# Kernel tuning notes

Hardware: AMD Instinct MI355X
Metric: run time of the kernel (lower is better)

The kernel has to match this reference:

```python
import jax, jax.numpy as jnp
import numpy as np

B, N, D = 256, 133, 1024
H, C = 8, 128  # per-head channels; H*C == out_channels
NEG_SLOPE = 0.2


def setup_inputs() -> dict:
    key = jax.random.key(0)
    kx, kw, ka, kadj = jax.random.split(key, 4)
    x = jax.random.normal(kx, (B, N, D), dtype=jnp.float32)
    W = jax.random.normal(kw, (H * C, D), dtype=jnp.float32) * 0.02  # nn.Linear weight (out,in)
    attn_w = jax.random.normal(ka, (2 * C,), dtype=jnp.float32) * 0.02  # attn Linear(2C,1) weight
    # binary adjacency with self-loops so every softmax column has a valid entry
    bern = (jax.random.uniform(kadj, (N, N)) < 0.15).astype(jnp.float32)
    adj = jnp.maximum(bern, jnp.eye(N, dtype=jnp.float32))[:, :, None]  # (N,N,1)
    return {"x": x, "W": W, "attn_w": attn_w, "adj": adj}


def reference(x, W, attn_w, adj):
    b, n, _ = x.shape
    g = (x @ W.T).reshape(b, n, H, C)  # (B,N,H,C)
    # concat(g_j, g_i) @ attn_w == g_j @ wl + g_i @ wr (leakyrelu applied after the sum)
    wl, wr = attn_w[:C], attn_w[C:]
    sj = jnp.einsum('bnhc,c->bnh', g, wl)  # score contribution from g[b, j]
    si = jnp.einsum('bnhc,c->bnh', g, wr)  # score contribution from g[b, i]
    e = jax.nn.leaky_relu(si[:, :, None, :] + sj[:, None, :, :], NEG_SLOPE)  # (B,N,N,H) e[b,i,j,h]
    e = jnp.where(adj[None] == 0, -jnp.inf, e)
    a = jax.nn.softmax(e, axis=1)  # faithful to original: softmax over dim=1 (the i axis)
    # dropout omitted (inference/eval mode)
    out = jnp.einsum('bijh,bjhf->bihf', a, g)  # aggregate over j
    return out.reshape(b, n, H * C)  # is_concat=True
```

## Files before the change

kernel.cpp:

```cpp
#include <hip/hip_runtime.h>

#define NB    133
#define NBP   136
#define BATCH 256
#define HEADS 8
#define CDIM  128
#define DDIM  1024
#define MROWS (BATCH * NB)
#define NDIM  (HEADS * CDIM)
#define BH    (BATCH * HEADS)

typedef __bf16 bf16_t;
typedef bf16_t bf16x8 __attribute__((ext_vector_type(8)));
typedef float  f32x4  __attribute__((ext_vector_type(4)));

__device__ __forceinline__ unsigned short f2bf(float f) {
  unsigned u = __float_as_uint(f);
  u += 0x7fffu + ((u >> 16) & 1u);
  return (unsigned short)(u >> 16);
}
__device__ __forceinline__ void load_lds16(const void* g, void* l) {
  __builtin_amdgcn_global_load_lds(
      (__attribute__((address_space(1))) void*)(g),
      (__attribute__((address_space(3))) void*)(l), 16, 0, 0);
}

__global__ __launch_bounds__(256) void cvt_kernel(const float* __restrict__ x,
                                                  const float* __restrict__ W,
                                                  unsigned short* __restrict__ xb,
                                                  unsigned short* __restrict__ wb) {
  const int nx = MROWS * DDIM / 8, nw = NDIM * DDIM / 8;
  int i = blockIdx.x * 256 + threadIdx.x;
  const float* src; unsigned short* dst; int k;
  if (i < nx)           { src = x; dst = xb; k = i; }
  else if (i < nx + nw) { src = W; dst = wb; k = i - nx; }
  else return;
  const float4* s4 = (const float4*)src;
  float4 a = s4[(size_t)k * 2];
  float4 b = s4[(size_t)k * 2 + 1];
  union { unsigned short u[8]; uint4 v; } p;
  p.u[0] = f2bf(a.x); p.u[1] = f2bf(a.y); p.u[2] = f2bf(a.z); p.u[3] = f2bf(a.w);
  p.u[4] = f2bf(b.x); p.u[5] = f2bf(b.y); p.u[6] = f2bf(b.z); p.u[7] = f2bf(b.w);
  ((uint4*)dst)[k] = p.v;
}

__global__ __launch_bounds__(192) void mask_kernel(const float* __restrict__ adj,
                                                   unsigned* __restrict__ rm,
                                                   unsigned* __restrict__ cm) {
  const int tid = threadIdx.x, lane = tid & 63, wv = tid >> 6, blk = blockIdx.x;
  if (blk < 144) {
    const int i = blk;
    bool on = (i < NB) && (tid < NB) && (adj[i * NB + tid] != 0.f);
    unsigned long long bb = __ballot(on);
    if (lane == 0)  rm[i * 6 + wv * 2]     = (unsigned)bb;
    if (lane == 32) rm[i * 6 + wv * 2 + 1] = (unsigned)(bb >> 32);
  } else {
    const int j = blk - 144;
    bool on = (tid < NB) && (adj[tid * NB + j] != 0.f);
    unsigned long long bb = __ballot(on);
    if (lane == 0)  cm[j * 6 + wv * 2]     = (unsigned)bb;
    if (lane == 32) cm[j * 6 + wv * 2 + 1] = (unsigned)(bb >> 32);
  }
}

__global__ __launch_bounds__(256) void gemm_kernel(const unsigned short* __restrict__ xb,
                                                   const unsigned short* __restrict__ wb,
                                                   const float* __restrict__ attn_w,
                                                   unsigned short* __restrict__ gb,
                                                   float* __restrict__ si_ws,
                                                   float* __restrict__ sj_ws) {
  __shared__ __attribute__((aligned(16))) unsigned short As[128 * 32];
  __shared__ __attribute__((aligned(16))) unsigned short Bs[128 * 32];
  __shared__ float sred[2][4][64];
  const int tid = threadIdx.x;
  const int h = blockIdx.x & 7, bm = blockIdx.x >> 3;
  const int lane = tid & 63, w = tid >> 6;
  const int wm = (w & 1) * 64, wn = (w >> 1) * 64;
  const int q = lane >> 4, li = lane & 15;
  const int c0 = tid, c1 = tid + 256;

  f32x4 acc[4][4] = {};
  const unsigned short* Ab = xb + (size_t)bm * 128 * DDIM;
  const unsigned short* Bb = wb + (size_t)h * 128 * DDIM;

  for (int kt = 0; kt < 32; ++kt) {
    const int k0 = kt * 32;
    load_lds16(Ab + (size_t)(c0 >> 2) * DDIM + k0 + (((c0 & 3) ^ ((c0 >> 3) & 3)) * 8), &As[c0 * 8]);
    load_lds16(Ab + (size_t)(c1 >> 2) * DDIM + k0 + (((c1 & 3) ^ ((c1 >> 3) & 3)) * 8), &As[c1 * 8]);
    load_lds16(Bb + (size_t)(c0 >> 2) * DDIM + k0 + (((c0 & 3) ^ ((c0 >> 3) & 3)) * 8), &Bs[c0 * 8]);
    load_lds16(Bb + (size_t)(c1 >> 2) * DDIM + k0 + (((c1 & 3) ^ ((c1 >> 3) & 3)) * 8), &Bs[c1 * 8]);
    __syncthreads();

    bf16x8 af[4], bfr[4];
    const int sub = (q ^ ((li >> 1) & 3)) * 8;
#pragma unroll
    for (int mi = 0; mi < 4; ++mi)
      af[mi] = *(const bf16x8*)&As[(wm + mi * 16 + li) * 32 + sub];
#pragma unroll
    for (int ni = 0; ni < 4; ++ni)
      bfr[ni] = *(const bf16x8*)&Bs[(wn + ni * 16 + li) * 32 + sub];
#pragma unroll
    for (int mi = 0; mi < 4; ++mi)
#pragma unroll
      for (int ni = 0; ni < 4; ++ni)
        acc[mi][ni] = __builtin_amdgcn_mfma_f32_16x16x32_bf16(af[mi], bfr[ni], acc[mi][ni], 0, 0, 0);
    __syncthreads();
  }

  float wl[4], wr[4];
#pragma unroll
  for (int ni = 0; ni < 4; ++ni) {
    wl[ni] = attn_w[wn + ni * 16 + li];
    wr[ni] = attn_w[CDIM + wn + ni * 16 + li];
  }
#pragma unroll
  for (int mi = 0; mi < 4; ++mi)
#pragma unroll
    for (int rr = 0; rr < 4; ++rr) {
      float pj = 0.f, pi = 0.f;
#pragma unroll
      for (int ni = 0; ni < 4; ++ni) {
        pj += acc[mi][ni][rr] * wl[ni];
        pi += acc[mi][ni][rr] * wr[ni];
      }
#pragma unroll
      for (int d = 1; d < 16; d <<= 1) {
        pj += __shfl_xor(pj, d);
        pi += __shfl_xor(pi, d);
      }
      if (li == 0) {
        sred[0][w][mi * 16 + q * 4 + rr] = pj;
        sred[1][w][mi * 16 + q * 4 + rr] = pi;
      }
    }
  __syncthreads();
  {
    const int row = tid & 127;
    const int which = tid >> 7;
    const int wlo = (row >> 6) & 1;
    const float v = sred[which][wlo][row & 63] + sred[which][wlo + 2][row & 63];
    const int rg = bm * 128 + row;
    const int b = rg / NB, n = rg - b * NB;
    float* dst = which ? si_ws : sj_ws;
    dst[(b * HEADS + h) * NB + n] = v;
  }

#pragma unroll
  for (int mi = 0; mi < 4; ++mi)
#pragma unroll
    for (int ni = 0; ni < 4; ++ni) {
      const int col = h * 128 + wn + ni * 16 + li;
      const size_t row0 = (size_t)(bm * 128 + wm + mi * 16 + q * 4);
#pragma unroll
      for (int rr = 0; rr < 4; ++rr)
        gb[(row0 + rr) * NDIM + col] = f2bf(acc[mi][ni][rr]);
    }
}

__global__ __launch_bounds__(192) void stats_kernel(const float* __restrict__ si_ws,
                                                    const float* __restrict__ sj_ws,
                                                    const unsigned* __restrict__ cm,
                                                    float2* __restrict__ smrg) {
  __shared__ float siL[NB];
  const int tid = threadIdx.x;
  const int base = blockIdx.x * NB;
  if (tid < NB) siL[tid] = si_ws[base + tid];
  __syncthreads();
  if (tid >= 160) return;
  float2 o = {0.f, 0.f};
  if (tid < NB) {
    const int j = tid;
    const float sjv = sj_ws[base + j];
    float m = -3.0e38f;
#pragma unroll
    for (int wd = 0; wd < 5; ++wd) {
      unsigned bits = cm[j * 6 + wd];
      while (bits) {
        const int i = __ffs(bits) - 1; bits &= bits - 1;
        float e = siL[wd * 32 + i] + sjv;
        e = e > 0.f ? e : 0.2f * e;
        m = fmaxf(m, e);
      }
    }
    float s = 0.f;
#pragma unroll
    for (int wd = 0; wd < 5; ++wd) {
      unsigned bits = cm[j * 6 + wd];
      while (bits) {
        const int i = __ffs(bits) - 1; bits &= bits - 1;
        float e = siL[wd * 32 + i] + sjv;
        e = e > 0.f ? e : 0.2f * e;
        s += __expf(e - m);
      }
    }
    o.x = sjv;
    o.y = m + __logf(s);
  }
  smrg[(size_t)blockIdx.x * 160 + tid] = o;
}

__global__ __launch_bounds__(256) void agg_kernel(const unsigned short* __restrict__ gb,
                                                  const float* __restrict__ si_ws,
                                                  const float2* __restrict__ smrg,
                                                  const unsigned* __restrict__ rm,
                                                  float* __restrict__ out) {
  __shared__ __attribute__((aligned(16))) unsigned short gTl[64 * NBP + 32];
  __shared__ __attribute__((aligned(8))) float2 smrL[160];
  const int tid = threadIdx.x;
  const int bh = blockIdx.x >> 1, fh = blockIdx.x & 1;
  const int b = bh >> 3, h = bh & 7;
  const int base = bh * NB;

  if (tid < 64) {
    gTl[tid * NBP + 133] = 0;
    *(unsigned*)&gTl[tid * NBP + 134] = 0;
  }
  if (tid >= 64 && tid < 80) *(unsigned*)&gTl[64 * NBP + 2 * (tid - 64)] = 0;
  if (tid < 160) smrL[tid] = smrg[(size_t)bh * 160 + tid];

  const unsigned short* gsrc = gb + (size_t)(b * NB) * NDIM + h * CDIM + fh * 64;
  for (int u = tid; u < NB * 16; u += 256) {
    const int j = u >> 4, fg = u & 15;
    const uint2 d = *(const uint2*)(gsrc + (size_t)j * NDIM + fg * 4);
    const int f0 = fg * 4;
    gTl[(f0 + 0) * NBP + j] = (unsigned short)(d.x);
    gTl[(f0 + 1) * NBP + j] = (unsigned short)(d.x >> 16);
    gTl[(f0 + 2) * NBP + j] = (unsigned short)(d.y);
    gTl[(f0 + 3) * NBP + j] = (unsigned short)(d.y >> 16);
  }
  __syncthreads();

  const int lane = tid & 63, wv = tid >> 6, q = lane >> 4, li = lane & 15;
  for (int mt = wv; mt < 9; mt += 4) {
    const int il = mt * 16 + li;
    const float si_r = si_ws[base + (il < NB ? il : NB - 1)];
    const unsigned* rmr = rm + il * 6;
    f32x4 acc[4] = {};
#pragma unroll
    for (int ks = 0; ks < 5; ++ks) {
      const int j0 = ks * 32 + q * 8;
      const unsigned bits = rmr[ks] >> (q * 8);
      bf16x8 afv;
#pragma unroll
      for (int jj = 0; jj < 8; ++jj) {
        const float2 sv = smrL[j0 + jj];
        float e = si_r + sv.x;
        e = e > 0.f ? e : 0.2f * e;
        const float wgt = ((bits >> jj) & 1u) ? __expf(e - sv.y) : 0.f;
        afv[jj] = (bf16_t)wgt;
      }
#pragma unroll
      for (int n = 0; n < 4; ++n) {
        const bf16x8 bv = *(const bf16x8*)&gTl[(n * 16 + li) * NBP + j0];
        acc[n] = __builtin_amdgcn_mfma_f32_16x16x32_bf16(afv, bv, acc[n], 0, 0, 0);
      }
    }
    float* obase = out + (size_t)(b * NB) * NDIM + h * CDIM + fh * 64;
#pragma unroll
    for (int n = 0; n < 4; ++n)
#pragma unroll
      for (int rr = 0; rr < 4; ++rr) {
        const int i = mt * 16 + q * 4 + rr;
        if (i < NB) obase[(size_t)i * NDIM + n * 16 + li] = acc[n][rr];
      }
  }
}

extern "C" void kernel_launch(void* const* d_in, const int* in_sizes, int n_in,
                              void* d_out, int out_size, void* d_ws, size_t ws_size,
                              hipStream_t stream) {
  const float* x      = (const float*)d_in[0];
  const float* W      = (const float*)d_in[1];
  const float* attn_w = (const float*)d_in[2];
  const float* adj    = (const float*)d_in[3];
  float* out = (float*)d_out;
  char* ws = (char*)d_ws;

  unsigned short* xb = (unsigned short*)(ws + 0);
  unsigned short* wb = (unsigned short*)(ws + 69730304);
  unsigned short* gb = (unsigned short*)(ws + 71827456);
  float* si = (float*)(ws + 141557760);
  float* sj = (float*)(ws + 142647296);
  unsigned* rm = (unsigned*)(ws + 143736832);
  unsigned* cm = (unsigned*)(ws + 143740288);
  float2* smrg = (float2*)(ws + 0);

  const int ncvt = (MROWS * DDIM + NDIM * DDIM) / 8;
  cvt_kernel<<<(ncvt + 255) / 256, 256, 0, stream>>>(x, W, xb, wb);
  mask_kernel<<<277, 192, 0, stream>>>(adj, rm, cm);
  gemm_kernel<<<266 * 8, 256, 0, stream>>>(xb, wb, attn_w, gb, si, sj);
  stats_kernel<<<BH, 192, 0, stream>>>(si, sj, cm, smrg);
  agg_kernel<<<BH * 2, 256, 0, stream>>>(gb, si, smrg, rm, out);
}
```

Measured before the change: 461.3 us.

## Use 256x256 GEMM tiles with a 4-stage async LDS pipeline

The projection GEMM now uses 256x256 output tiles computed by 512-thread blocks, with each block covering two heads. A four-buffer LDS ring is filled through direct global-to-LDS loads, issued three stages ahead and gated by explicit vmcnt waits and raw barriers. MFMA sections run at raised wave priority. The aim is more data reuse per tile and overlap of global loads with matrix math. The cost is about 136KB of LDS per block, which likely allows only one block per CU, and a grid of 532 large blocks that may leave a partial last wave.

```diff
diff --git a/kernel.cpp b/kernel.cpp
--- a/kernel.cpp
+++ b/kernel.cpp
@@ -9,6 +9,7 @@
 #define MROWS (BATCH * NB)
 #define NDIM  (HEADS * CDIM)
 #define BH    (BATCH * HEADS)
+#define NT    32
 
 typedef __bf16 bf16_t;
 typedef bf16_t bf16x8 __attribute__((ext_vector_type(8)));
@@ -24,6 +25,12 @@
       (__attribute__((address_space(1))) void*)(g),
       (__attribute__((address_space(3))) void*)(l), 16, 0, 0);
 }
+__device__ __forceinline__ void bar() {
+  asm volatile("" ::: "memory");
+  __builtin_amdgcn_s_barrier();
+  asm volatile("" ::: "memory");
+}
+#define VMWAIT(n) asm volatile("s_waitcnt vmcnt(" #n ")" ::: "memory")
 
 __global__ __launch_bounds__(256) void cvt_kernel(const float* __restrict__ x,
                                                   const float* __restrict__ W,
@@ -63,65 +70,89 @@
   }
 }
 
-__global__ __launch_bounds__(256) void gemm_kernel(const unsigned short* __restrict__ xb,
-                                                   const unsigned short* __restrict__ wb,
-                                                   const float* __restrict__ attn_w,
-                                                   unsigned short* __restrict__ gb,
-                                                   float* __restrict__ si_ws,
-                                                   float* __restrict__ sj_ws) {
-  __shared__ __attribute__((aligned(16))) unsigned short As[128 * 32];
-  __shared__ __attribute__((aligned(16))) unsigned short Bs[128 * 32];
-  __shared__ float sred[2][4][64];
+__global__ __launch_bounds__(512, 2) void gemm_kernel(const unsigned short* __restrict__ xb,
+                                                      const unsigned short* __restrict__ wb,
+                                                      const float* __restrict__ attn_w,
+                                                      unsigned short* __restrict__ gb,
+                                                      float* __restrict__ si_ws,
+                                                      float* __restrict__ sj_ws) {
+  __shared__ __attribute__((aligned(16))) unsigned short lds[4][2][8192];
+  __shared__ float sred[2][8][128];
+
   const int tid = threadIdx.x;
-  const int h = blockIdx.x & 7, bm = blockIdx.x >> 3;
+  const int bn = blockIdx.x & 3, bm = blockIdx.x >> 2;
   const int lane = tid & 63, w = tid >> 6;
-  const int wm = (w & 1) * 64, wn = (w >> 1) * 64;
+  const int wr = w >> 2, wc = w & 3;
   const int q = lane >> 4, li = lane & 15;
-  const int c0 = tid, c1 = tid + 256;
-
-  f32x4 acc[4][4] = {};
-  const unsigned short* Ab = xb + (size_t)bm * 128 * DDIM;
-  const unsigned short* Bb = wb + (size_t)h * 128 * DDIM;
-
-  for (int kt = 0; kt < 32; ++kt) {
-    const int k0 = kt * 32;
-    load_lds16(Ab + (size_t)(c0 >> 2) * DDIM + k0 + (((c0 & 3) ^ ((c0 >> 3) & 3)) * 8), &As[c0 * 8]);
-    load_lds16(Ab + (size_t)(c1 >> 2) * DDIM + k0 + (((c1 & 3) ^ ((c1 >> 3) & 3)) * 8), &As[c1 * 8]);
-    load_lds16(Bb + (size_t)(c0 >> 2) * DDIM + k0 + (((c0 & 3) ^ ((c0 >> 3) & 3)) * 8), &Bs[c0 * 8]);
-    load_lds16(Bb + (size_t)(c1 >> 2) * DDIM + k0 + (((c1 & 3) ^ ((c1 >> 3) & 3)) * 8), &Bs[c1 * 8]);
-    __syncthreads();
-
-    bf16x8 af[4], bfr[4];
-    const int sub = (q ^ ((li >> 1) & 3)) * 8;
-#pragma unroll
-    for (int mi = 0; mi < 4; ++mi)
-      af[mi] = *(const bf16x8*)&As[(wm + mi * 16 + li) * 32 + sub];
-#pragma unroll
-    for (int ni = 0; ni < 4; ++ni)
-      bfr[ni] = *(const bf16x8*)&Bs[(wn + ni * 16 + li) * 32 + sub];
-#pragma unroll
-    for (int mi = 0; mi < 4; ++mi)
-#pragma unroll
-      for (int ni = 0; ni < 4; ++ni)
-        acc[mi][ni] = __builtin_amdgcn_mfma_f32_16x16x32_bf16(af[mi], bfr[ni], acc[mi][ni], 0, 0, 0);
-    __syncthreads();
-  }
-
-  float wl[4], wr[4];
+  const int sub = (q ^ ((li >> 1) & 3)) * 8;
+
+  const unsigned short* Ab = xb + (size_t)bm * 256 * DDIM;
+  const unsigned short* Bb = wb + (size_t)bn * 256 * DDIM;
+
+  const int u0 = tid, u1 = tid + 512;
+  const size_t sa0 = (size_t)(u0 >> 2) * DDIM + (((u0 & 3) ^ ((u0 >> 3) & 3)) * 8);
+  const size_t sa1 = (size_t)(u1 >> 2) * DDIM + (((u1 & 3) ^ ((u1 >> 3) & 3)) * 8);
+
+  f32x4 acc[8][4] = {};
+
+#define STAGE(T) do { \
+    unsigned short* _la = &lds[(T) & 3][0][0]; \
+    unsigned short* _lb = &lds[(T) & 3][1][0]; \
+    const int _k = (T) * 32; \
+    load_lds16(Ab + sa0 + _k, _la + u0 * 8); \
+    load_lds16(Ab + sa1 + _k, _la + u1 * 8); \
+    load_lds16(Bb + sa0 + _k, _lb + u0 * 8); \
+    load_lds16(Bb + sa1 + _k, _lb + u1 * 8); \
+  } while (0)
+
+#define COMPUTE(T) do { \
+    const unsigned short* _as = &lds[(T) & 3][0][0]; \
+    const unsigned short* _bs = &lds[(T) & 3][1][0]; \
+    bf16x8 af[8], bfr[4]; \
+    _Pragma("unroll") \
+    for (int mi = 0; mi < 8; ++mi) \
+      af[mi] = *(const bf16x8*)&_as[(wr * 128 + mi * 16 + li) * 32 + sub]; \
+    _Pragma("unroll") \
+    for (int ni = 0; ni < 4; ++ni) \
+      bfr[ni] = *(const bf16x8*)&_bs[(wc * 64 + ni * 16 + li) * 32 + sub]; \
+    __builtin_amdgcn_s_setprio(1); \
+    _Pragma("unroll") \
+    for (int mi = 0; mi < 8; ++mi) \
+      _Pragma("unroll") \
+      for (int ni = 0; ni < 4; ++ni) \
+        acc[mi][ni] = __builtin_amdgcn_mfma_f32_16x16x32_bf16(af[mi], bfr[ni], acc[mi][ni], 0, 0, 0); \
+    __builtin_amdgcn_s_setprio(0); \
+  } while (0)
+
+  STAGE(0); STAGE(1); STAGE(2);
+  VMWAIT(8);
+  bar();
+  for (int t = 0; t < NT - 3; ++t) {
+    STAGE(t + 3);
+    COMPUTE(t);
+    VMWAIT(8);
+    bar();
+  }
+  COMPUTE(NT - 3); VMWAIT(4); bar();
+  COMPUTE(NT - 2); VMWAIT(0); bar();
+  COMPUTE(NT - 1);
+
+  float wlv[4], wrv[4];
 #pragma unroll
   for (int ni = 0; ni < 4; ++ni) {
-    wl[ni] = attn_w[wn + ni * 16 + li];
-    wr[ni] = attn_w[CDIM + wn + ni * 16 + li];
-  }
-#pragma unroll
-  for (int mi = 0; mi < 4; ++mi)
+    const int cc = (wc & 1) * 64 + ni * 16 + li;
+    wlv[ni] = attn_w[cc];
+    wrv[ni] = attn_w[CDIM + cc];
+  }
+#pragma unroll
+  for (int mi = 0; mi < 8; ++mi)
 #pragma unroll
     for (int rr = 0; rr < 4; ++rr) {
       float pj = 0.f, pi = 0.f;
 #pragma unroll
       for (int ni = 0; ni < 4; ++ni) {
-        pj += acc[mi][ni][rr] * wl[ni];
-        pi += acc[mi][ni][rr] * wr[ni];
+        pj += acc[mi][ni][rr] * wlv[ni];
+        pi += acc[mi][ni][rr] * wrv[ni];
       }
 #pragma unroll
       for (int d = 1; d < 16; d <<= 1) {
@@ -134,27 +165,33 @@
       }
     }
   __syncthreads();
-  {
-    const int row = tid & 127;
-    const int which = tid >> 7;
-    const int wlo = (row >> 6) & 1;
-    const float v = sred[which][wlo][row & 63] + sred[which][wlo + 2][row & 63];
-    const int rg = bm * 128 + row;
+#pragma unroll
+  for (int idx0 = 0; idx0 < 2; ++idx0) {
+    const int idx = idx0 * 512 + tid;
+    const int row = idx & 255;
+    const int hw = (idx >> 8) & 1;
+    const int which = idx >> 9;
+    const int wb2 = (row >> 7) * 4 + hw * 2;
+    const float v = sred[which][wb2][row & 127] + sred[which][wb2 + 1][row & 127];
+    const int rg = bm * 256 + row;
     const int b = rg / NB, n = rg - b * NB;
+    const int h = bn * 2 + hw;
     float* dst = which ? si_ws : sj_ws;
     dst[(b * HEADS + h) * NB + n] = v;
   }
 
 #pragma unroll
-  for (int mi = 0; mi < 4; ++mi)
+  for (int mi = 0; mi < 8; ++mi)
 #pragma unroll
     for (int ni = 0; ni < 4; ++ni) {
-      const int col = h * 128 + wn + ni * 16 + li;
-      const size_t row0 = (size_t)(bm * 128 + wm + mi * 16 + q * 4);
+      const int col = bn * 256 + wc * 64 + ni * 16 + li;
+      const size_t row0 = (size_t)(bm * 256 + wr * 128 + mi * 16 + q * 4);
 #pragma unroll
       for (int rr = 0; rr < 4; ++rr)
         gb[(row0 + rr) * NDIM + col] = f2bf(acc[mi][ni][rr]);
     }
+#undef STAGE
+#undef COMPUTE
 }
 
 __global__ __launch_bounds__(192) void stats_kernel(const float* __restrict__ si_ws,
@@ -288,7 +325,7 @@
   const int ncvt = (MROWS * DDIM + NDIM * DDIM) / 8;
   cvt_kernel<<<(ncvt + 255) / 256, 256, 0, stream>>>(x, W, xb, wb);
   mask_kernel<<<277, 192, 0, stream>>>(adj, rm, cm);
-  gemm_kernel<<<266 * 8, 256, 0, stream>>>(xb, wb, attn_w, gb, si, sj);
+  gemm_kernel<<<133 * 4, 512, 0, stream>>>(xb, wb, attn_w, gb, si, sj);
   stats_kernel<<<BH, 192, 0, stream>>>(si, sj, cm, smrg);
   agg_kernel<<<BH * 2, 256, 0, stream>>>(gb, si, smrg, rm, out);
 }
```

Result: slower. 472.0 us (+2.3%).

## Restructure projection GEMM with 128x256 tiles and triple-buffered LDS pipeline

Applied to the files above, without the earlier changes.

The projection GEMM now computes 128x256 output tiles, covering two heads per block, instead of 128x128 tiles. It stages A and B tiles through a three-deep LDS ring using async global-to-LDS loads with explicit vmcnt waits and raw barriers, and splits the MFMA work into two halves so loads overlap compute. It also remaps block IDs to group blocks that share an A tile, raises wave priority around MFMA bursts, and adjusts the LDS swizzle. The aim is to hide global load latency and raise reuse per loaded A tile. The cost is more LDS and registers, with occupancy bounded to 2 blocks per CU, and the hand-managed wait counts are fragile.

```diff
diff --git a/kernel.cpp b/kernel.cpp
--- a/kernel.cpp
+++ b/kernel.cpp
@@ -9,6 +9,7 @@
 #define MROWS (BATCH * NB)
 #define NDIM  (HEADS * CDIM)
 #define BH    (BATCH * HEADS)
+#define NKT   32
 
 typedef __bf16 bf16_t;
 typedef bf16_t bf16x8 __attribute__((ext_vector_type(8)));
@@ -24,6 +25,12 @@
       (__attribute__((address_space(1))) void*)(g),
       (__attribute__((address_space(3))) void*)(l), 16, 0, 0);
 }
+__device__ __forceinline__ void bar() {
+  asm volatile("" ::: "memory");
+  __builtin_amdgcn_s_barrier();
+  asm volatile("" ::: "memory");
+}
+#define VMWAIT(n) asm volatile("s_waitcnt vmcnt(" #n ")" ::: "memory")
 
 __global__ __launch_bounds__(256) void cvt_kernel(const float* __restrict__ x,
                                                   const float* __restrict__ W,
@@ -63,65 +70,114 @@
   }
 }
 
-__global__ __launch_bounds__(256) void gemm_kernel(const unsigned short* __restrict__ xb,
-                                                   const unsigned short* __restrict__ wb,
-                                                   const float* __restrict__ attn_w,
-                                                   unsigned short* __restrict__ gb,
-                                                   float* __restrict__ si_ws,
-                                                   float* __restrict__ sj_ws) {
-  __shared__ __attribute__((aligned(16))) unsigned short As[128 * 32];
-  __shared__ __attribute__((aligned(16))) unsigned short Bs[128 * 32];
-  __shared__ float sred[2][4][64];
+__global__ __launch_bounds__(256, 2) void gemm_kernel(const unsigned short* __restrict__ xb,
+                                                      const unsigned short* __restrict__ wb,
+                                                      const float* __restrict__ attn_w,
+                                                      unsigned short* __restrict__ gb,
+                                                      float* __restrict__ si_ws,
+                                                      float* __restrict__ sj_ws) {
+  __shared__ __attribute__((aligned(16))) unsigned short Abuf[3][128 * 32];
+  __shared__ __attribute__((aligned(16))) unsigned short Bbuf[3][256 * 32];
+  __shared__ float sred[2][4][128];
+
   const int tid = threadIdx.x;
-  const int h = blockIdx.x & 7, bm = blockIdx.x >> 3;
+  const int orig = blockIdx.x;
+  const int wg = (orig & 7) * 133 + (orig >> 3);
+  const int bn = wg & 3, bm = wg >> 2;
+
   const int lane = tid & 63, w = tid >> 6;
-  const int wm = (w & 1) * 64, wn = (w >> 1) * 64;
   const int q = lane >> 4, li = lane & 15;
-  const int c0 = tid, c1 = tid + 256;
-
-  f32x4 acc[4][4] = {};
+
   const unsigned short* Ab = xb + (size_t)bm * 128 * DDIM;
-  const unsigned short* Bb = wb + (size_t)h * 128 * DDIM;
-
-  for (int kt = 0; kt < 32; ++kt) {
-    const int k0 = kt * 32;
-    load_lds16(Ab + (size_t)(c0 >> 2) * DDIM + k0 + (((c0 & 3) ^ ((c0 >> 3) & 3)) * 8), &As[c0 * 8]);
-    load_lds16(Ab + (size_t)(c1 >> 2) * DDIM + k0 + (((c1 & 3) ^ ((c1 >> 3) & 3)) * 8), &As[c1 * 8]);
-    load_lds16(Bb + (size_t)(c0 >> 2) * DDIM + k0 + (((c0 & 3) ^ ((c0 >> 3) & 3)) * 8), &Bs[c0 * 8]);
-    load_lds16(Bb + (size_t)(c1 >> 2) * DDIM + k0 + (((c1 & 3) ^ ((c1 >> 3) & 3)) * 8), &Bs[c1 * 8]);
-    __syncthreads();
-
-    bf16x8 af[4], bfr[4];
-    const int sub = (q ^ ((li >> 1) & 3)) * 8;
-#pragma unroll
-    for (int mi = 0; mi < 4; ++mi)
-      af[mi] = *(const bf16x8*)&As[(wm + mi * 16 + li) * 32 + sub];
-#pragma unroll
-    for (int ni = 0; ni < 4; ++ni)
-      bfr[ni] = *(const bf16x8*)&Bs[(wn + ni * 16 + li) * 32 + sub];
-#pragma unroll
-    for (int mi = 0; mi < 4; ++mi)
-#pragma unroll
-      for (int ni = 0; ni < 4; ++ni)
-        acc[mi][ni] = __builtin_amdgcn_mfma_f32_16x16x32_bf16(af[mi], bfr[ni], acc[mi][ni], 0, 0, 0);
-    __syncthreads();
-  }
-
-  float wl[4], wr[4];
+  const unsigned short* Bb = wb + (size_t)bn * 256 * DDIM;
+
+  int sA[2], sB[4];
+#pragma unroll
+  for (int i = 0; i < 2; ++i) {
+    const int f = tid + i * 256;
+    sA[i] = (f >> 2) * DDIM + (((f & 3) ^ ((f >> 2) & 3)) << 3);
+  }
+#pragma unroll
+  for (int i = 0; i < 4; ++i) {
+    const int f = tid + i * 256;
+    sB[i] = (f >> 2) * DDIM + (((f & 3) ^ ((f >> 2) & 3)) << 3);
+  }
+#define STGA(buf_, kt_) do { \
+    load_lds16(Ab + sA[0] + (kt_) * 32, &Abuf[buf_][tid * 8]); \
+    load_lds16(Ab + sA[1] + (kt_) * 32, &Abuf[buf_][(tid + 256) * 8]); \
+  } while (0)
+#define STGB(buf_, kt_) do { \
+    load_lds16(Bb + sB[0] + (kt_) * 32, &Bbuf[buf_][tid * 8]); \
+    load_lds16(Bb + sB[1] + (kt_) * 32, &Bbuf[buf_][(tid + 256) * 8]); \
+    load_lds16(Bb + sB[2] + (kt_) * 32, &Bbuf[buf_][(tid + 512) * 8]); \
+    load_lds16(Bb + sB[3] + (kt_) * 32, &Bbuf[buf_][(tid + 768) * 8]); \
+  } while (0)
+
+  const int asl = (q ^ (li & 3)) << 3;
+
+  f32x4 acc[8][4] = {};
+  bf16x8 a[8], bf01[2], bf23[2];
+
+  STGA(0, 0); STGB(0, 0);
+  STGA(1, 1); STGB(1, 1);
+  VMWAIT(6);
+  bar();
+
+  for (int t = 0; t < NKT; ++t) {
+    const int cur = t % 3, nxt = (t + 2) % 3;
+    const unsigned short* As = &Abuf[cur][0];
+    const unsigned short* Bs = &Bbuf[cur][0];
+#pragma unroll
+    for (int mi = 0; mi < 8; ++mi)
+      a[mi] = *(const bf16x8*)&As[(mi * 16 + li) * 32 + asl];
+#pragma unroll
+    for (int ni = 0; ni < 2; ++ni)
+      bf01[ni] = *(const bf16x8*)&Bs[(w * 64 + ni * 16 + li) * 32 + asl];
+    bar();
+    __builtin_amdgcn_s_setprio(1);
+#pragma unroll
+    for (int mi = 0; mi < 8; ++mi)
+#pragma unroll
+      for (int ni = 0; ni < 2; ++ni)
+        acc[mi][ni] = __builtin_amdgcn_mfma_f32_16x16x32_bf16(a[mi], bf01[ni], acc[mi][ni], 0, 0, 0);
+    __builtin_amdgcn_s_setprio(0);
+#pragma unroll
+    for (int ni = 0; ni < 2; ++ni)
+      bf23[ni] = *(const bf16x8*)&Bs[(w * 64 + (ni + 2) * 16 + li) * 32 + asl];
+    if (t < NKT - 2) {
+      STGA(nxt, t + 2); STGB(nxt, t + 2);
+      VMWAIT(6);
+    } else {
+      VMWAIT(0);
+    }
+    bar();
+    __builtin_amdgcn_s_setprio(1);
+#pragma unroll
+    for (int mi = 0; mi < 8; ++mi)
+#pragma unroll
+      for (int ni = 0; ni < 2; ++ni)
+        acc[mi][ni + 2] = __builtin_amdgcn_mfma_f32_16x16x32_bf16(a[mi], bf23[ni], acc[mi][ni + 2], 0, 0, 0);
+    __builtin_amdgcn_s_setprio(0);
+  }
+#undef STGA
+#undef STGB
+
+  float wlv[4], wrv[4];
 #pragma unroll
   for (int ni = 0; ni < 4; ++ni) {
-    wl[ni] = attn_w[wn + ni * 16 + li];
-    wr[ni] = attn_w[CDIM + wn + ni * 16 + li];
-  }
-#pragma unroll
-  for (int mi = 0; mi < 4; ++mi)
+    const int cc = (w & 1) * 64 + ni * 16 + li;
+    wlv[ni] = attn_w[cc];
+    wrv[ni] = attn_w[CDIM + cc];
+  }
+#pragma unroll
+  for (int mi = 0; mi < 8; ++mi)
 #pragma unroll
     for (int rr = 0; rr < 4; ++rr) {
       float pj = 0.f, pi = 0.f;
 #pragma unroll
       for (int ni = 0; ni < 4; ++ni) {
-        pj += acc[mi][ni][rr] * wl[ni];
-        pi += acc[mi][ni][rr] * wr[ni];
+        pj += acc[mi][ni][rr] * wlv[ni];
+        pi += acc[mi][ni][rr] * wrv[ni];
       }
 #pragma unroll
       for (int d = 1; d < 16; d <<= 1) {
@@ -134,23 +190,26 @@
       }
     }
   __syncthreads();
-  {
-    const int row = tid & 127;
-    const int which = tid >> 7;
-    const int wlo = (row >> 6) & 1;
-    const float v = sred[which][wlo][row & 63] + sred[which][wlo + 2][row & 63];
+#pragma unroll
+  for (int idx0 = 0; idx0 < 2; ++idx0) {
+    const int idx = idx0 * 256 + tid;
+    const int row = idx & 127;
+    const int hw = (idx >> 7) & 1;
+    const int which = idx >> 8;
+    const float v = sred[which][hw * 2][row] + sred[which][hw * 2 + 1][row];
     const int rg = bm * 128 + row;
     const int b = rg / NB, n = rg - b * NB;
+    const int h = bn * 2 + hw;
     float* dst = which ? si_ws : sj_ws;
     dst[(b * HEADS + h) * NB + n] = v;
   }
 
 #pragma unroll
-  for (int mi = 0; mi < 4; ++mi)
+  for (int mi = 0; mi < 8; ++mi)
 #pragma unroll
     for (int ni = 0; ni < 4; ++ni) {
-      const int col = h * 128 + wn + ni * 16 + li;
-      const size_t row0 = (size_t)(bm * 128 + wm + mi * 16 + q * 4);
+      const int col = bn * 256 + w * 64 + ni * 16 + li;
+      const size_t row0 = (size_t)(bm * 128 + mi * 16 + q * 4);
 #pragma unroll
       for (int rr = 0; rr < 4; ++rr)
         gb[(row0 + rr) * NDIM + col] = f2bf(acc[mi][ni][rr]);
@@ -288,7 +347,7 @@
   const int ncvt = (MROWS * DDIM + NDIM * DDIM) / 8;
   cvt_kernel<<<(ncvt + 255) / 256, 256, 0, stream>>>(x, W, xb, wb);
   mask_kernel<<<277, 192, 0, stream>>>(adj, rm, cm);
-  gemm_kernel<<<266 * 8, 256, 0, stream>>>(xb, wb, attn_w, gb, si, sj);
+  gemm_kernel<<<266 * 4, 256, 0, stream>>>(xb, wb, attn_w, gb, si, sj);
   stats_kernel<<<BH, 192, 0, stream>>>(si, sj, cm, smrg);
   agg_kernel<<<BH * 2, 256, 0, stream>>>(gb, si, smrg, rm, out);
 }
```

Measured after the change: 437.3 us. 5.2% less time.
